# Kernel tuning notes

Hardware: AMD Instinct MI355X
Metric: run time of the kernel (lower is better)

Reference implementation:

```python
import jax, jax.numpy as jnp
import numpy as np

# Model constants (match init_kwargs / torchcde conventions)
B = 1024        # batch
L = 128         # number of spline knots (grid_points = 0..L-1)
C_IN = 8        # input_channels
HID = 64        # hidden_channels
MLP_H = 128     # CDEFunc hidden width
INIT_H = 20     # initial-network hidden width


def setup_inputs() -> dict:
    key = jax.random.key(0)
    ks = jax.random.split(key, 9)
    # cubic spline coeffs: (B, L-1, 4*C_IN) laid out as [a, b, c, d] per interval
    coeffs = jax.random.normal(ks[0], (B, L - 1, 4 * C_IN), dtype=jnp.float32) * 0.1
    # initial network: C_IN -> 20 -> HID (ReLU, then Tanh)
    Wi1 = jax.random.normal(ks[1], (C_IN, INIT_H), dtype=jnp.float32) / np.sqrt(C_IN)
    bi1 = jnp.zeros((INIT_H,), jnp.float32)
    Wi2 = jax.random.normal(ks[2], (INIT_H, HID), dtype=jnp.float32) / np.sqrt(INIT_H)
    bi2 = jnp.zeros((HID,), jnp.float32)
    # CDE vector field: (HID+1) -> 128 -> C_IN*HID (ReLU, then Tanh)
    W1 = jax.random.normal(ks[3], (HID + 1, MLP_H), dtype=jnp.float32) / np.sqrt(HID + 1)
    b1 = jnp.zeros((MLP_H,), jnp.float32)
    W2 = jax.random.normal(ks[4], (MLP_H, C_IN * HID), dtype=jnp.float32) / np.sqrt(MLP_H)
    b2 = jnp.zeros((C_IN * HID,), jnp.float32)
    return {"coeffs": coeffs, "Wi1": Wi1, "bi1": bi1, "Wi2": Wi2, "bi2": bi2,
            "W1": W1, "b1": b1, "W2": W2, "b2": b2}


def reference(coeffs, Wi1, bi1, Wi2, bi2, W1, b1, W2, b2):
    Lm1 = coeffs.shape[1]
    # a,b,c,d: each (B, L-1, C_IN). X(t) = a + b*f + c*f^2 + d*f^3 on interval idx,
    # dX/dt = b + 2c*f + 3d*f^2, with f = t - idx (torchcde CubicSpline convention).
    a, b, c, d = jnp.split(coeffs, 4, axis=-1)

    def dXdt(t):
        idx = jnp.clip(jnp.floor(t).astype(jnp.int32), 0, Lm1 - 1)
        fr = t - idx
        return b[:, idx] + 2.0 * c[:, idx] * fr + 3.0 * d[:, idx] * fr * fr  # (B, C_IN)

    def cde_func(t, z):
        # FFN([HID+1, 128, C_IN*HID], ReLU hidden, Tanh output) on concat(t, z)
        tz = jnp.concatenate([jnp.full((z.shape[0], 1), t, z.dtype), z], axis=1)
        h = jax.nn.relu(tz @ W1 + b1)
        return jnp.tanh(h @ W2 + b2).reshape(z.shape[0], HID, C_IN)  # (B, HID, C_IN)

    def vf(t, z):
        # dz/dt = f(t,z) @ dX/dt
        return jnp.einsum('bhc,bc->bh', cde_func(t, z), dXdt(t))

    # z0 = initial(X(t0)); X(0) = a at interval 0 with frac 0
    X0 = a[:, 0]
    z0 = jnp.tanh(jax.nn.relu(X0 @ Wi1 + bi1) @ Wi2 + bi2)  # (B, HID)

    def rk4_step(z, i):
        t = i.astype(z.dtype)
        k1 = vf(t, z)
        k2 = vf(t + 0.5, z + 0.5 * k1)
        k3 = vf(t + 0.5, z + 0.5 * k2)
        k4 = vf(t + 1.0, z + k3)
        z_new = z + (k1 + 2.0 * k2 + 2.0 * k3 + k4) / 6.0
        return z_new, z_new

    _, zs = jax.lax.scan(rk4_step, z0, jnp.arange(Lm1))  # (L-1, B, HID)
    # z evaluated at all grid points, like cdeint(t=X.grid_points): (B, L, HID)
    return jnp.concatenate([z0[None], zs], axis=0).transpose(1, 0, 2)
```

## Files before the change

### kernel.cpp

```cpp
#include <hip/hip_runtime.h>
#include <stdint.h>

#define LM1  127
#define NTHR 1024

typedef _Float16 half8_t __attribute__((ext_vector_type(8)));
typedef float    f32x4   __attribute__((ext_vector_type(4)));

__device__ __forceinline__ float fast_tanh(float x) {
  float e = __expf(2.0f * x);
  return 1.0f - 2.0f * __builtin_amdgcn_rcpf(e + 1.0f);
}

__global__ void __launch_bounds__(NTHR, 4) cde_kernel(
    const float* __restrict__ coeffs,
    const float* __restrict__ Wi1, const float* __restrict__ bi1,
    const float* __restrict__ Wi2, const float* __restrict__ bi2,
    const float* __restrict__ W1,  const float* __restrict__ b1,
    const float* __restrict__ W2,  const float* __restrict__ b2,
    float* __restrict__ out)
{
  __shared__ __align__(16) _Float16 zsb[1024];
  __shared__ __align__(16) _Float16 hA [2048];
  __shared__ __align__(16) float    fwb[8][288];
  __shared__ __align__(16) float    gds[2][3][4][8];

  const int t    = threadIdx.x;
  const int lane = t & 63;
  const int w    = t >> 6;
  const int l15  = lane & 15;
  const int lq   = lane >> 4;
  const int row0 = blockIdx.x * 4;
  const int wc   = w & 7;

  for (int u = t; u < 512;  u += NTHR) ((uint32_t*)zsb)[u] = 0u;
  for (int u = t; u < 1024; u += NTHR) ((uint32_t*)hA)[u]  = 0u;

  half8_t bB[2] = {};
  float w1t_c = 0.f, b1_c = 0.f;
  _Float16* hwp = &hA[0];
  if (w >= 8) {
    const int wb = w - 8;
    #pragma unroll
    for (int kt = 0; kt < 2; ++kt)
      #pragma unroll
      for (int j = 0; j < 8; ++j)
        bB[kt][j] = (_Float16)W1[(1 + kt * 32 + lq * 8 + j) * 128 + wb * 16 + l15];
    w1t_c = W1[wb * 16 + l15];
    b1_c  = b1[wb * 16 + l15];
    const int col = 16 * wb + l15;
    const int ktw = (col >> 5) & 3, lqw2 = (col >> 3) & 3, j2 = col & 7;
    hwp = &hA[8 * (ktw * 64 + lqw2 * 16) + j2];
  }

  half8_t bf[4][4] = {};
  if (w < 8) {
    #pragma unroll
    for (int nt = 0; nt < 4; ++nt)
      #pragma unroll
      for (int kt = 0; kt < 4; ++kt)
        #pragma unroll
        for (int j = 0; j < 8; ++j)
          bf[nt][kt][j] =
              (_Float16)W2[(kt * 32 + lq * 8 + j) * 512 + w * 64 + nt * 16 + l15];
  }

  const int r_ = lane & 3;
  const int hh = (lane >> 2) & 7;
  const int cp = lane >> 5;
  float b2c0 = 0.f, b2c1 = 0.f, b2c2 = 0.f, b2c3 = 0.f;
  if (w < 8) {
    const float* bp = b2 + w * 64 + hh * 8 + cp * 4;
    b2c0 = bp[0]; b2c1 = bp[1]; b2c2 = bp[2]; b2c3 = bp[3];
  }
  const int frbase = 36 * hh + 16 * cp + r_;
  const int hx = 8 * wc + hh;

  _Float16* zwp;
  {
    const int kh = hx >> 5, lqw = (hx >> 3) & 3, jj = hx & 7;
    zwp = &zsb[8 * (kh * 64 + lqw * 16 + r_) + jj];
  }
  float* const fsp = &fwb[wc][36 * (l15 >> 3) + 4 * (l15 & 7)];

  float z = 0.0f;
  if (w < 8 && lane < 32) {
    const float* cb = coeffs + (size_t)(row0 + r_) * (LM1 * 32);
    float x0[8];
    #pragma unroll
    for (int c = 0; c < 8; ++c) x0[c] = cb[c];
    float acc = bi2[hx];
    for (int j = 0; j < 20; ++j) {
      float u = bi1[j];
      #pragma unroll
      for (int c = 0; c < 8; ++c) u += x0[c] * Wi1[c * 20 + j];
      acc += fmaxf(u, 0.0f) * Wi2[j * 64 + hx];
    }
    z = fast_tanh(acc);
    out[(size_t)(row0 + r_) * 8192 + hx] = z;
  }

  const int rg = (lane >> 3) & 3, cg = lane & 7;
  const float* cbp = coeffs + (size_t)(row0 + rg) * (LM1 * 32);
  float pb = 0.f, pc = 0.f, pd = 0.f, pbn = 0.f;
  const bool stg = (w == 15) && (lane < 32);
  if (stg) { pb = cbp[8 + cg]; pc = cbp[16 + cg]; pd = cbp[24 + cg]; pbn = cbp[40 + cg]; }

  __syncthreads();

  for (int i = 0; i < LM1; ++i) {
    if (stg) {
      gds[i & 1][0][rg][cg] = pb;
      gds[i & 1][1][rg][cg] = pb + pc + 0.75f * pd;
      gds[i & 1][2][rg][cg] = (i < LM1 - 1) ? pbn : fmaf(3.0f, pd, fmaf(2.0f, pc, pb));
      if (i + 1 < LM1) {
        const float* nb = cbp + (size_t)(i + 1) * 32;
        pb = nb[8 + cg]; pc = nb[16 + cg]; pd = nb[24 + cg];
        pbn = (i + 2 < LM1) ? nb[40 + cg] : 0.0f;
      }
    }

    float ksum = 0.0f, kprev = 0.0f;
    #pragma unroll
    for (int s = 0; s < 4; ++s) {
      const float coef = (s == 0) ? 0.0f : (s == 3) ? 1.0f : 0.5f;
      const float ts   = (float)i + ((s == 0) ? 0.0f : (s == 3) ? 1.0f : 0.5f);
      const int   gi   = (s == 0) ? 0 : (s == 3) ? 2 : 1;

      if (w < 8 && lane < 32) *zwp = (_Float16)(z + coef * kprev);
      __syncthreads();

      if (w >= 8) {
        const half8_t a0 = *(const half8_t*)(zsb + 8 * lane);
        const half8_t a1 = *(const half8_t*)(zsb + 512 + 8 * lane);
        f32x4 hd = {0.f, 0.f, 0.f, 0.f};
        hd = __builtin_amdgcn_mfma_f32_16x16x32_f16(a0, bB[0], hd, 0, 0, 0);
        hd = __builtin_amdgcn_mfma_f32_16x16x32_f16(a1, bB[1], hd, 0, 0, 0);
        if (lane < 16) {
          const float hb = fmaf(ts, w1t_c, b1_c);
          hwp[0]  = (_Float16)fmaxf(hd.x + hb, 0.0f);
          hwp[8]  = (_Float16)fmaxf(hd.y + hb, 0.0f);
          hwp[16] = (_Float16)fmaxf(hd.z + hb, 0.0f);
          hwp[24] = (_Float16)fmaxf(hd.w + hb, 0.0f);
        }
      }
      __syncthreads();

      if (w < 8) {
        half8_t ha[4];
        #pragma unroll
        for (int kt = 0; kt < 4; ++kt)
          ha[kt] = *(const half8_t*)(hA + 512 * kt + 8 * lane);
        f32x4 d0 = {0.f, 0.f, 0.f, 0.f}, d1 = d0, d2 = d0, d3 = d0;
        #pragma unroll
        for (int kt = 0; kt < 4; ++kt) {
          d0 = __builtin_amdgcn_mfma_f32_16x16x32_f16(ha[kt], bf[0][kt], d0, 0, 0, 0);
          d1 = __builtin_amdgcn_mfma_f32_16x16x32_f16(ha[kt], bf[1][kt], d1, 0, 0, 0);
          d2 = __builtin_amdgcn_mfma_f32_16x16x32_f16(ha[kt], bf[2][kt], d2, 0, 0, 0);
          d3 = __builtin_amdgcn_mfma_f32_16x16x32_f16(ha[kt], bf[3][kt], d3, 0, 0, 0);
        }
        if (lane < 16) {
          *(f32x4*)(fsp)       = d0;
          *(f32x4*)(fsp + 72)  = d1;
          *(f32x4*)(fsp + 144) = d2;
          *(f32x4*)(fsp + 216) = d3;
        }
        asm volatile("s_waitcnt lgkmcnt(0)" ::: "memory");

        const float* fb = &fwb[wc][frbase];
        const float v0 = fb[0], v1 = fb[4], v2 = fb[8], v3 = fb[12];
        const f32x4 gv = *(const f32x4*)&gds[i & 1][gi][r_][4 * cp];
        float kcv = fast_tanh(v0 + b2c0) * gv.x + fast_tanh(v1 + b2c1) * gv.y
                  + fast_tanh(v2 + b2c2) * gv.z + fast_tanh(v3 + b2c3) * gv.w;
        kcv += __shfl_xor(kcv, 32, 64);
        kprev = kcv;
        ksum += ((s == 1 || s == 2) ? 2.0f : 1.0f) * kcv;
      }
    }
    if (w < 8 && lane < 32) {
      z += ksum * (1.0f / 6.0f);
      out[(size_t)(row0 + r_) * 8192 + (size_t)(i + 1) * 64 + hx] = z;
    }
  }
}

extern "C" void kernel_launch(void* const* d_in, const int* in_sizes, int n_in,
                              void* d_out, int out_size, void* d_ws, size_t ws_size,
                              hipStream_t stream) {
  const float* coeffs = (const float*)d_in[0];
  const float* Wi1    = (const float*)d_in[1];
  const float* bi1    = (const float*)d_in[2];
  const float* Wi2    = (const float*)d_in[3];
  const float* bi2    = (const float*)d_in[4];
  const float* W1     = (const float*)d_in[5];
  const float* b1     = (const float*)d_in[6];
  const float* W2     = (const float*)d_in[7];
  const float* b2     = (const float*)d_in[8];
  float* out          = (float*)d_out;
  (void)in_sizes; (void)n_in; (void)out_size; (void)d_ws; (void)ws_size;
  cde_kernel<<<256, NTHR, 0, stream>>>(coeffs, Wi1, bi1, Wi2, bi2,
                                       W1, b1, W2, b2, out);
}
```

Baseline: 567.3 us.

## Merge layer-1 and layer-2 warp roles into one 8-wave block

Shrinks the block from 16 waves to 8, and each wave now computes both the first-layer MFMA (hidden activations) and its slice of the second layer, instead of having separate producer and consumer wave groups. This removes idle waves during each RK stage and cuts the barrier participant count. It also replaces the cross-half shuffle with v_permlane32_swap and hoists the gds load earlier. Each wave now holds both weight sets in registers, which raises register pressure, and the two layers now run serially within each wave instead of on separate wave groups.

```diff
diff --git a/kernel.cpp b/kernel.cpp
--- a/kernel.cpp
+++ b/kernel.cpp
@@ -2,7 +2,7 @@
 #include <stdint.h>
 
 #define LM1  127
-#define NTHR 1024
+#define NTHR 512
 
 typedef _Float16 half8_t __attribute__((ext_vector_type(8)));
 typedef float    f32x4   __attribute__((ext_vector_type(4)));
@@ -12,7 +12,7 @@
   return 1.0f - 2.0f * __builtin_amdgcn_rcpf(e + 1.0f);
 }
 
-__global__ void __launch_bounds__(NTHR, 4) cde_kernel(
+__global__ void __launch_bounds__(NTHR, 2) cde_kernel(
     const float* __restrict__ coeffs,
     const float* __restrict__ Wi1, const float* __restrict__ bi1,
     const float* __restrict__ Wi2, const float* __restrict__ bi2,
@@ -31,60 +31,52 @@
   const int l15  = lane & 15;
   const int lq   = lane >> 4;
   const int row0 = blockIdx.x * 4;
-  const int wc   = w & 7;
 
   for (int u = t; u < 512;  u += NTHR) ((uint32_t*)zsb)[u] = 0u;
   for (int u = t; u < 1024; u += NTHR) ((uint32_t*)hA)[u]  = 0u;
 
-  half8_t bB[2] = {};
-  float w1t_c = 0.f, b1_c = 0.f;
-  _Float16* hwp = &hA[0];
-  if (w >= 8) {
-    const int wb = w - 8;
-    #pragma unroll
-    for (int kt = 0; kt < 2; ++kt)
+  half8_t bB[2];
+  #pragma unroll
+  for (int kt = 0; kt < 2; ++kt)
+    #pragma unroll
+    for (int j = 0; j < 8; ++j)
+      bB[kt][j] = (_Float16)W1[(1 + kt * 32 + lq * 8 + j) * 128 + w * 16 + l15];
+  const float w1t_c = W1[w * 16 + l15];
+  const float b1_c  = b1[w * 16 + l15];
+  _Float16* hwp;
+  {
+    const int col = 16 * w + l15;
+    const int ktw = (col >> 5) & 3, lqw2 = (col >> 3) & 3, j2 = col & 7;
+    hwp = &hA[8 * (ktw * 64 + lqw2 * 16) + j2];
+  }
+
+  half8_t bf[4][4];
+  #pragma unroll
+  for (int nt = 0; nt < 4; ++nt)
+    #pragma unroll
+    for (int kt = 0; kt < 4; ++kt)
       #pragma unroll
       for (int j = 0; j < 8; ++j)
-        bB[kt][j] = (_Float16)W1[(1 + kt * 32 + lq * 8 + j) * 128 + wb * 16 + l15];
-    w1t_c = W1[wb * 16 + l15];
-    b1_c  = b1[wb * 16 + l15];
-    const int col = 16 * wb + l15;
-    const int ktw = (col >> 5) & 3, lqw2 = (col >> 3) & 3, j2 = col & 7;
-    hwp = &hA[8 * (ktw * 64 + lqw2 * 16) + j2];
-  }
-
-  half8_t bf[4][4] = {};
-  if (w < 8) {
-    #pragma unroll
-    for (int nt = 0; nt < 4; ++nt)
-      #pragma unroll
-      for (int kt = 0; kt < 4; ++kt)
-        #pragma unroll
-        for (int j = 0; j < 8; ++j)
-          bf[nt][kt][j] =
-              (_Float16)W2[(kt * 32 + lq * 8 + j) * 512 + w * 64 + nt * 16 + l15];
-  }
+        bf[nt][kt][j] =
+            (_Float16)W2[(kt * 32 + lq * 8 + j) * 512 + w * 64 + nt * 16 + l15];
 
   const int r_ = lane & 3;
   const int hh = (lane >> 2) & 7;
   const int cp = lane >> 5;
-  float b2c0 = 0.f, b2c1 = 0.f, b2c2 = 0.f, b2c3 = 0.f;
-  if (w < 8) {
-    const float* bp = b2 + w * 64 + hh * 8 + cp * 4;
-    b2c0 = bp[0]; b2c1 = bp[1]; b2c2 = bp[2]; b2c3 = bp[3];
-  }
+  const float* bp = b2 + w * 64 + hh * 8 + cp * 4;
+  const float b2c0 = bp[0], b2c1 = bp[1], b2c2 = bp[2], b2c3 = bp[3];
   const int frbase = 36 * hh + 16 * cp + r_;
-  const int hx = 8 * wc + hh;
+  const int hx = 8 * w + hh;
 
   _Float16* zwp;
   {
     const int kh = hx >> 5, lqw = (hx >> 3) & 3, jj = hx & 7;
     zwp = &zsb[8 * (kh * 64 + lqw * 16 + r_) + jj];
   }
-  float* const fsp = &fwb[wc][36 * (l15 >> 3) + 4 * (l15 & 7)];
+  float* const fsp = &fwb[w][36 * (l15 >> 3) + 4 * (l15 & 7)];
 
   float z = 0.0f;
-  if (w < 8 && lane < 32) {
+  if (lane < 32) {
     const float* cb = coeffs + (size_t)(row0 + r_) * (LM1 * 32);
     float x0[8];
     #pragma unroll
@@ -103,7 +95,7 @@
   const int rg = (lane >> 3) & 3, cg = lane & 7;
   const float* cbp = coeffs + (size_t)(row0 + rg) * (LM1 * 32);
   float pb = 0.f, pc = 0.f, pd = 0.f, pbn = 0.f;
-  const bool stg = (w == 15) && (lane < 32);
+  const bool stg = (w == 7) && (lane < 32);
   if (stg) { pb = cbp[8 + cg]; pc = cbp[16 + cg]; pd = cbp[24 + cg]; pbn = cbp[40 + cg]; }
 
   __syncthreads();
@@ -127,10 +119,10 @@
       const float ts   = (float)i + ((s == 0) ? 0.0f : (s == 3) ? 1.0f : 0.5f);
       const int   gi   = (s == 0) ? 0 : (s == 3) ? 2 : 1;
 
-      if (w < 8 && lane < 32) *zwp = (_Float16)(z + coef * kprev);
+      if (lane < 32) *zwp = (_Float16)(z + coef * kprev);
       __syncthreads();
 
-      if (w >= 8) {
+      {
         const half8_t a0 = *(const half8_t*)(zsb + 8 * lane);
         const half8_t a1 = *(const half8_t*)(zsb + 512 + 8 * lane);
         f32x4 hd = {0.f, 0.f, 0.f, 0.f};
@@ -146,7 +138,9 @@
       }
       __syncthreads();
 
-      if (w < 8) {
+      {
+        const f32x4 gv = *(const f32x4*)&gds[i & 1][gi][r_][4 * cp];
+
         half8_t ha[4];
         #pragma unroll
         for (int kt = 0; kt < 4; ++kt)
@@ -167,17 +161,20 @@
         }
         asm volatile("s_waitcnt lgkmcnt(0)" ::: "memory");
 
-        const float* fb = &fwb[wc][frbase];
+        const float* fb = &fwb[w][frbase];
         const float v0 = fb[0], v1 = fb[4], v2 = fb[8], v3 = fb[12];
-        const f32x4 gv = *(const f32x4*)&gds[i & 1][gi][r_][4 * cp];
         float kcv = fast_tanh(v0 + b2c0) * gv.x + fast_tanh(v1 + b2c1) * gv.y
                   + fast_tanh(v2 + b2c2) * gv.z + fast_tanh(v3 + b2c3) * gv.w;
-        kcv += __shfl_xor(kcv, 32, 64);
+        {
+          int a = __float_as_int(kcv), b = a;
+          asm volatile("v_permlane32_swap_b32 %0, %1" : "+v"(a), "+v"(b));
+          kcv = __int_as_float(a) + __int_as_float(b);
+        }
         kprev = kcv;
         ksum += ((s == 1 || s == 2) ? 2.0f : 1.0f) * kcv;
       }
     }
-    if (w < 8 && lane < 32) {
+    if (lane < 32) {
       z += ksum * (1.0f / 6.0f);
       out[(size_t)(row0 + r_) * 8192 + (size_t)(i + 1) * 64 + hx] = z;
     }
```

Result: faster. 540.3 us (-4.8%).
